# Kernel optimization log

Measured on AMD Instinct MI355X. Metric: run time of the kernel, lower is better.

Reference implementation:

```python
import jax, jax.numpy as jnp
import numpy as np

L, P = 16384, 512
DT_MIN, DT_MAX = 0.001, 0.1
THRESHOLD = 1.0  # spike threshold assumed for cartesian_spike


def setup_inputs() -> dict:
    key = jax.random.key(0)
    k1, k2, k3, k4, k5, k6 = jax.random.split(key, 6)
    u = jax.random.normal(k1, (L, P), dtype=jnp.float32)
    # Stored Lambda param: [..., 0] = log(-Re(Lambda)) with Re(Lambda) < 0, [..., 1] = Im(Lambda)
    lam_real_neg = jax.random.uniform(k2, (P,), minval=0.1, maxval=1.0)  # -Re(Lambda)
    lam_imag = jax.random.normal(k3, (P,)) * 3.0
    Lambda = jnp.stack([jnp.log(lam_real_neg), lam_imag], axis=-1).astype(jnp.float32)
    # init_log_steps: log(dt) uniform in [log(dt_min), log(dt_max)], shape (P, 1)
    log_step = (np.log(DT_MIN) + jax.random.uniform(k4, (P, 1)) * (np.log(DT_MAX) - np.log(DT_MIN))).astype(jnp.float32)
    V_re = jax.random.normal(k5, (P, P), dtype=jnp.float32) / np.sqrt(P)
    V_im = jax.random.normal(k6, (P, P), dtype=jnp.float32) / np.sqrt(P)
    return {"u": u, "Lambda": Lambda, "log_step": log_step, "V_re": V_re, "V_im": V_im}


def _binop(q_i, q_j):
    A_i, b_i = q_i
    A_j, b_j = q_j
    return (A_j * A_i, A_j * b_i + b_j)


def reference(u, Lambda, log_step, V_re, V_im):
    # keep_imag = False: u stays real. discretization = 'zoh', activation = 'cartesian_spike'.
    Lambda_tilde = -jnp.exp(Lambda[..., 0]) + 1j * Lambda[..., 1]            # (P,) complex
    step = jnp.exp(log_step[:, 0])                                            # (P,)
    Lambda_bar = jnp.exp(Lambda_tilde * step)                                 # (P,) |.|<1
    # B_tilde = I, so zoh gives B_bar = diag((Lambda_bar - 1)/Lambda); B_bar @ u_t = coef * u_t
    B_coef = (Lambda_bar - 1.0) / Lambda_tilde                                # (P,)
    Lambda_elements = jnp.broadcast_to(Lambda_bar, (u.shape[0], Lambda_bar.shape[0]))
    Bu_elements = B_coef[None, :] * u.astype(Lambda_bar.dtype)                # (L, P) complex
    _, xs = jax.lax.associative_scan(_binop, (Lambda_elements, Bu_elements))  # (L, P)
    V = V_re + 1j * V_im
    xs = xs @ V.T                                                             # vmap(V @ x) over L
    spikes = (xs.real > THRESHOLD).astype(jnp.float32)                        # cartesian_spike
    return spikes
```

## Files before the change

kernel.cpp:

```cpp
#include <hip/hip_runtime.h>

#define L_LEN   16384
#define P_DIM   512
#define CHUNK   64
#define NCHUNK  256

#define KDIM    1024
#define NDIM    512
#define BM      128
#define BN      128
#define BK      64

typedef __bf16 bf16_t;
typedef __bf16 bf16x8 __attribute__((ext_vector_type(8)));
typedef float  floatx4 __attribute__((ext_vector_type(4)));

__device__ __forceinline__ void channel_consts(const float* __restrict__ Lam,
                                               const float* __restrict__ lstep,
                                               int p, float& ar, float& ai,
                                               float& br, float& bi) {
    float lr = -expf(Lam[2 * p + 0]);
    float li = Lam[2 * p + 1];
    float s  = expf(lstep[p]);
    float er = expf(lr * s);
    ar = er * cosf(li * s);
    ai = er * sinf(li * s);
    float dr = ar - 1.0f, di = ai;
    float inv = 1.0f / (lr * lr + li * li);
    br = (dr * lr + di * li) * inv;
    bi = (di * lr - dr * li) * inv;
}

__global__ void __launch_bounds__(P_DIM) k_scan_ends(const float* __restrict__ u,
        const float* __restrict__ Lam, const float* __restrict__ lstep,
        float2* __restrict__ endv) {
    int p = threadIdx.x;
    int c = blockIdx.x;
    float ar, ai, br, bi;
    channel_consts(Lam, lstep, p, ar, ai, br, bi);
    float xr = 0.f, xi = 0.f;
    const float* up = u + (size_t)c * CHUNK * P_DIM + p;
    #pragma unroll 8
    for (int k = 0; k < CHUNK; ++k) {
        float uv = up[(size_t)k * P_DIM];
        float nr = ar * xr - ai * xi + br * uv;
        float ni = ar * xi + ai * xr + bi * uv;
        xr = nr; xi = ni;
    }
    endv[(size_t)c * P_DIM + p] = make_float2(xr, xi);
}

__global__ void __launch_bounds__(1024) k_carry(const float* __restrict__ Lam,
        const float* __restrict__ lstep, const float2* __restrict__ endv,
        float2* __restrict__ carry) {
    __shared__ float2 zl[4 * (NCHUNK + 2)];
    int tid = threadIdx.x;
    int g = tid & 3;
    int c = tid >> 2;
    int p = blockIdx.x * 4 + g;
    int zi_base = g * (NCHUNK + 2);

    float lr = -expf(Lam[2 * p + 0]);
    float li = Lam[2 * p + 1];
    float s  = expf(lstep[p]);
    float t  = s * (float)CHUNK;
    float er = expf(lr * t);
    float Ar = er * cosf(li * t);
    float Ai = er * sinf(li * t);

    float2 e = endv[(size_t)c * P_DIM + p];
    float zr = e.x, zi = e.y;
    zl[zi_base + c] = make_float2(zr, zi);
    __syncthreads();
    for (int st = 1; st < NCHUNK; st <<= 1) {
        float tr = 0.f, ti = 0.f;
        if (c >= st) { float2 v = zl[zi_base + c - st]; tr = v.x; ti = v.y; }
        __syncthreads();
        zr += Ar * tr - Ai * ti;
        zi += Ar * ti + Ai * tr;
        zl[zi_base + c] = make_float2(zr, zi);
        float nAr = Ar * Ar - Ai * Ai;
        float nAi = 2.f * Ar * Ai;
        Ar = nAr; Ai = nAi;
        __syncthreads();
    }
    float2 cv = make_float2(0.f, 0.f);
    if (c > 0) cv = zl[zi_base + c - 1];
    carry[(size_t)c * P_DIM + p] = cv;
}

__global__ void __launch_bounds__(P_DIM) k_materialize(const float* __restrict__ u,
        const float* __restrict__ Lam, const float* __restrict__ lstep,
        const float2* __restrict__ carry, bf16_t* __restrict__ A) {
    int p = threadIdx.x;
    int c = blockIdx.x;
    float ar, ai, br, bi;
    channel_consts(Lam, lstep, p, ar, ai, br, bi);
    float2 x0 = carry[(size_t)c * P_DIM + p];
    float xr = x0.x, xi = x0.y;
    const float* up = u + (size_t)c * CHUNK * P_DIM + p;
    uint32_t* Ap = (uint32_t*)(A + (size_t)c * CHUNK * KDIM) + p;
    #pragma unroll 4
    for (int k = 0; k < CHUNK; ++k) {
        float uv = up[(size_t)k * P_DIM];
        float nr = ar * xr - ai * xi + br * uv;
        float ni = ar * xi + ai * xr + bi * uv;
        xr = nr; xi = ni;
        bf16_t hr = (bf16_t)xr, hi = (bf16_t)xi;
        uint32_t pk = (uint32_t)__builtin_bit_cast(unsigned short, hr)
                    | ((uint32_t)__builtin_bit_cast(unsigned short, hi) << 16);
        Ap[(size_t)k * (KDIM / 2)] = pk;
    }
}

__global__ void __launch_bounds__(256) k_bt(const float* __restrict__ Vre,
        const float* __restrict__ Vim, bf16_t* __restrict__ Bt) {
    int idx = blockIdx.x * 256 + threadIdx.x;
    bf16_t r = (bf16_t)Vre[idx];
    bf16_t m = (bf16_t)(-Vim[idx]);
    uint32_t pk = (uint32_t)__builtin_bit_cast(unsigned short, r)
                | ((uint32_t)__builtin_bit_cast(unsigned short, m) << 16);
    ((uint32_t*)Bt)[idx] = pk;
}

__global__ void __launch_bounds__(256) k_gemm(const bf16_t* __restrict__ A,
        const bf16_t* __restrict__ Bt, float* __restrict__ out) {
    __shared__ uint4 As4[BM * BK * 2 / 16];
    __shared__ uint4 Bs4[BN * BK * 2 / 16];

    const int tid  = threadIdx.x;
    const int lane = tid & 63;
    const int w    = tid >> 6;
    const int m0   = blockIdx.x * BM;
    const int n0   = blockIdx.y * BN;
    const int wm   = (w >> 1) * 64;
    const int wn   = (w & 1) * 64;

    const int fr_m = lane & 15;
    const int fr_g = lane >> 4;

    floatx4 acc[4][4];
    #pragma unroll
    for (int i = 0; i < 4; ++i)
        #pragma unroll
        for (int j = 0; j < 4; ++j) {
            floatx4 z = {0.f, 0.f, 0.f, 0.f};
            acc[i][j] = z;
        }

    const bf16_t* Asrc = A  + (size_t)m0 * KDIM;
    const bf16_t* Bsrc = Bt + (size_t)n0 * KDIM;

    const bf16_t* ga[4]; const bf16_t* gb[4];
    char* la[4]; char* lb[4];
    #pragma unroll
    for (int i = 0; i < 4; ++i) {
        int q   = i * 256 + tid;
        int row = q >> 3;
        int gc  = (q & 7) ^ (row & 7);
        ga[i] = Asrc + (size_t)row * KDIM + gc * 8;
        gb[i] = Bsrc + (size_t)row * KDIM + gc * 8;
        la[i] = (char*)As4 + (size_t)q * 16;
        lb[i] = (char*)Bs4 + (size_t)q * 16;
    }

    for (int kt = 0; kt < KDIM; kt += BK) {
        __syncthreads();
        #pragma unroll
        for (int i = 0; i < 4; ++i) {
            __builtin_amdgcn_global_load_lds(
                (const __attribute__((address_space(1))) void*)(ga[i] + kt),
                (__attribute__((address_space(3))) void*)la[i], 16, 0, 0);
            __builtin_amdgcn_global_load_lds(
                (const __attribute__((address_space(1))) void*)(gb[i] + kt),
                (__attribute__((address_space(3))) void*)lb[i], 16, 0, 0);
        }
        __syncthreads();
        #pragma unroll
        for (int kk = 0; kk < BK; kk += 32) {
            bf16x8 af[4], bf[4];
            #pragma unroll
            for (int i = 0; i < 4; ++i) {
                int m  = wm + i * 16 + fr_m;
                int cc = (kk >> 3) + fr_g;
                int sc = cc ^ (m & 7);
                af[i] = *(const bf16x8*)((const bf16_t*)As4 + m * BK + sc * 8);
            }
            #pragma unroll
            for (int j = 0; j < 4; ++j) {
                int n  = wn + j * 16 + fr_m;
                int cc = (kk >> 3) + fr_g;
                int sc = cc ^ (n & 7);
                bf[j] = *(const bf16x8*)((const bf16_t*)Bs4 + n * BK + sc * 8);
            }
            #pragma unroll
            for (int i = 0; i < 4; ++i)
                #pragma unroll
                for (int j = 0; j < 4; ++j)
                    acc[i][j] = __builtin_amdgcn_mfma_f32_16x16x32_bf16(
                        af[i], bf[j], acc[i][j], 0, 0, 0);
        }
    }

    #pragma unroll
    for (int i = 0; i < 4; ++i)
        #pragma unroll
        for (int j = 0; j < 4; ++j)
            #pragma unroll
            for (int r = 0; r < 4; ++r) {
                int rr = wm + i * 16 + fr_g * 4 + r;
                int cl = wn + j * 16 + fr_m;
                float v = acc[i][j][r];
                out[(size_t)(m0 + rr) * NDIM + (n0 + cl)] = (v > 1.0f) ? 1.0f : 0.0f;
            }
}

extern "C" void kernel_launch(void* const* d_in, const int* in_sizes, int n_in,
                              void* d_out, int out_size, void* d_ws, size_t ws_size,
                              hipStream_t stream) {
    (void)in_sizes; (void)n_in; (void)out_size; (void)ws_size;
    const float* u     = (const float*)d_in[0];
    const float* Lam   = (const float*)d_in[1];
    const float* lstep = (const float*)d_in[2];
    const float* Vre   = (const float*)d_in[3];
    const float* Vim   = (const float*)d_in[4];
    float* out = (float*)d_out;

    char* ws = (char*)d_ws;
    const size_t endv_bytes  = (size_t)NCHUNK * P_DIM * sizeof(float2);
    const size_t carry_bytes = endv_bytes;
    const size_t bt_bytes    = (size_t)NDIM * KDIM * sizeof(bf16_t);
    float2* endv  = (float2*)(ws);
    float2* carry = (float2*)(ws + endv_bytes);
    bf16_t* Bt    = (bf16_t*)(ws + endv_bytes + carry_bytes);
    bf16_t* A     = (bf16_t*)(ws + endv_bytes + carry_bytes + bt_bytes);

    hipLaunchKernelGGL(k_scan_ends, dim3(NCHUNK), dim3(P_DIM), 0, stream,
                       u, Lam, lstep, endv);
    hipLaunchKernelGGL(k_bt, dim3(NDIM * P_DIM / 256), dim3(256), 0, stream,
                       Vre, Vim, Bt);
    hipLaunchKernelGGL(k_carry, dim3(P_DIM / 4), dim3(1024), 0, stream,
                       Lam, lstep, endv, carry);
    hipLaunchKernelGGL(k_materialize, dim3(NCHUNK), dim3(P_DIM), 0, stream,
                       u, Lam, lstep, carry, A);
    hipLaunchKernelGGL(k_gemm, dim3(L_LEN / BM, NDIM / BN), dim3(256), 0, stream,
                       A, Bt, out);
}
```

Baseline: 128.4 us.

## Fuse scan, carry, materialize and B prep into one cooperative kernel

Merges the chunk-end scan, the B-matrix bf16 packing, the cross-chunk carry propagation and the materialization into a single cooperative kernel that uses a grid-wide sync. The u chunk is held in registers so it is read once instead of twice. The log-depth shared-memory carry scan is replaced by a per-block serial loop over the preceding chunk ends. This removes three launches and one pass over u, but adds a grid barrier, a serial carry loop of up to 255 steps in later blocks, and heavy register use for the 64-element u buffer, which may lower occupancy.

Result: slower. 283.0 us (+120.4%).

```diff
diff --git a/kernel.cpp b/kernel.cpp
--- a/kernel.cpp
+++ b/kernel.cpp
@@ -1,4 +1,7 @@
 #include <hip/hip_runtime.h>
+#include <hip/hip_cooperative_groups.h>
+
+namespace cg = cooperative_groups;
 
 #define L_LEN   16384
 #define P_DIM   512
@@ -15,112 +18,77 @@
 typedef __bf16 bf16x8 __attribute__((ext_vector_type(8)));
 typedef float  floatx4 __attribute__((ext_vector_type(4)));
 
-__device__ __forceinline__ void channel_consts(const float* __restrict__ Lam,
-                                               const float* __restrict__ lstep,
-                                               int p, float& ar, float& ai,
-                                               float& br, float& bi) {
+__device__ __forceinline__ uint32_t pack_bf16(float a, float b) {
+    bf16_t ha = (bf16_t)a, hb = (bf16_t)b;
+    return (uint32_t)__builtin_bit_cast(unsigned short, ha)
+         | ((uint32_t)__builtin_bit_cast(unsigned short, hb) << 16);
+}
+
+__global__ void __launch_bounds__(P_DIM) k_scan_all(const float* __restrict__ u,
+        const float* __restrict__ Lam, const float* __restrict__ lstep,
+        const float* __restrict__ Vre, const float* __restrict__ Vim,
+        float2* __restrict__ endv, bf16_t* __restrict__ Bt,
+        bf16_t* __restrict__ A) {
+    const int p = threadIdx.x;
+    const int c = blockIdx.x;
+
+    {
+        int t = c * P_DIM + p;
+        float2 vr = ((const float2*)Vre)[t];
+        float2 vi = ((const float2*)Vim)[t];
+        uint2 pk = make_uint2(pack_bf16(vr.x, -vi.x), pack_bf16(vr.y, -vi.y));
+        ((uint2*)Bt)[t] = pk;
+    }
+
     float lr = -expf(Lam[2 * p + 0]);
     float li = Lam[2 * p + 1];
     float s  = expf(lstep[p]);
     float er = expf(lr * s);
-    ar = er * cosf(li * s);
-    ai = er * sinf(li * s);
+    float ar = er * cosf(li * s);
+    float ai = er * sinf(li * s);
     float dr = ar - 1.0f, di = ai;
     float inv = 1.0f / (lr * lr + li * li);
-    br = (dr * lr + di * li) * inv;
-    bi = (di * lr - dr * li) * inv;
-}
-
-__global__ void __launch_bounds__(P_DIM) k_scan_ends(const float* __restrict__ u,
-        const float* __restrict__ Lam, const float* __restrict__ lstep,
-        float2* __restrict__ endv) {
-    int p = threadIdx.x;
-    int c = blockIdx.x;
-    float ar, ai, br, bi;
-    channel_consts(Lam, lstep, p, ar, ai, br, bi);
+    float br = (dr * lr + di * li) * inv;
+    float bi = (di * lr - dr * li) * inv;
+    float tt = s * (float)CHUNK;
+    float eR = expf(lr * tt);
+    float Ar = eR * cosf(li * tt);
+    float Ai = eR * sinf(li * tt);
+
+    const float* up = u + (size_t)c * CHUNK * P_DIM + p;
+    float ur[CHUNK];
+    #pragma unroll
+    for (int k = 0; k < CHUNK; ++k) ur[k] = up[(size_t)k * P_DIM];
+
     float xr = 0.f, xi = 0.f;
-    const float* up = u + (size_t)c * CHUNK * P_DIM + p;
-    #pragma unroll 8
+    #pragma unroll
     for (int k = 0; k < CHUNK; ++k) {
-        float uv = up[(size_t)k * P_DIM];
-        float nr = ar * xr - ai * xi + br * uv;
-        float ni = ar * xi + ai * xr + bi * uv;
+        float nr = ar * xr - ai * xi + br * ur[k];
+        float ni = ar * xi + ai * xr + bi * ur[k];
         xr = nr; xi = ni;
     }
     endv[(size_t)c * P_DIM + p] = make_float2(xr, xi);
-}
-
-__global__ void __launch_bounds__(1024) k_carry(const float* __restrict__ Lam,
-        const float* __restrict__ lstep, const float2* __restrict__ endv,
-        float2* __restrict__ carry) {
-    __shared__ float2 zl[4 * (NCHUNK + 2)];
-    int tid = threadIdx.x;
-    int g = tid & 3;
-    int c = tid >> 2;
-    int p = blockIdx.x * 4 + g;
-    int zi_base = g * (NCHUNK + 2);
-
-    float lr = -expf(Lam[2 * p + 0]);
-    float li = Lam[2 * p + 1];
-    float s  = expf(lstep[p]);
-    float t  = s * (float)CHUNK;
-    float er = expf(lr * t);
-    float Ar = er * cosf(li * t);
-    float Ai = er * sinf(li * t);
-
-    float2 e = endv[(size_t)c * P_DIM + p];
-    float zr = e.x, zi = e.y;
-    zl[zi_base + c] = make_float2(zr, zi);
-    __syncthreads();
-    for (int st = 1; st < NCHUNK; st <<= 1) {
-        float tr = 0.f, ti = 0.f;
-        if (c >= st) { float2 v = zl[zi_base + c - st]; tr = v.x; ti = v.y; }
-        __syncthreads();
-        zr += Ar * tr - Ai * ti;
-        zi += Ar * ti + Ai * tr;
-        zl[zi_base + c] = make_float2(zr, zi);
-        float nAr = Ar * Ar - Ai * Ai;
-        float nAi = 2.f * Ar * Ai;
-        Ar = nAr; Ai = nAi;
-        __syncthreads();
-    }
-    float2 cv = make_float2(0.f, 0.f);
-    if (c > 0) cv = zl[zi_base + c - 1];
-    carry[(size_t)c * P_DIM + p] = cv;
-}
-
-__global__ void __launch_bounds__(P_DIM) k_materialize(const float* __restrict__ u,
-        const float* __restrict__ Lam, const float* __restrict__ lstep,
-        const float2* __restrict__ carry, bf16_t* __restrict__ A) {
-    int p = threadIdx.x;
-    int c = blockIdx.x;
-    float ar, ai, br, bi;
-    channel_consts(Lam, lstep, p, ar, ai, br, bi);
-    float2 x0 = carry[(size_t)c * P_DIM + p];
-    float xr = x0.x, xi = x0.y;
-    const float* up = u + (size_t)c * CHUNK * P_DIM + p;
+
+    __threadfence();
+    cg::this_grid().sync();
+
+    float cr = 0.f, ci = 0.f;
+    for (int j = 0; j < c; ++j) {
+        float2 e = endv[(size_t)j * P_DIM + p];
+        float nr = Ar * cr - Ai * ci + e.x;
+        float ni = Ar * ci + Ai * cr + e.y;
+        cr = nr; ci = ni;
+    }
+
+    xr = cr; xi = ci;
     uint32_t* Ap = (uint32_t*)(A + (size_t)c * CHUNK * KDIM) + p;
-    #pragma unroll 4
+    #pragma unroll
     for (int k = 0; k < CHUNK; ++k) {
-        float uv = up[(size_t)k * P_DIM];
-        float nr = ar * xr - ai * xi + br * uv;
-        float ni = ar * xi + ai * xr + bi * uv;
+        float nr = ar * xr - ai * xi + br * ur[k];
+        float ni = ar * xi + ai * xr + bi * ur[k];
         xr = nr; xi = ni;
-        bf16_t hr = (bf16_t)xr, hi = (bf16_t)xi;
-        uint32_t pk = (uint32_t)__builtin_bit_cast(unsigned short, hr)
-                    | ((uint32_t)__builtin_bit_cast(unsigned short, hi) << 16);
-        Ap[(size_t)k * (KDIM / 2)] = pk;
-    }
-}
-
-__global__ void __launch_bounds__(256) k_bt(const float* __restrict__ Vre,
-        const float* __restrict__ Vim, bf16_t* __restrict__ Bt) {
-    int idx = blockIdx.x * 256 + threadIdx.x;
-    bf16_t r = (bf16_t)Vre[idx];
-    bf16_t m = (bf16_t)(-Vim[idx]);
-    uint32_t pk = (uint32_t)__builtin_bit_cast(unsigned short, r)
-                | ((uint32_t)__builtin_bit_cast(unsigned short, m) << 16);
-    ((uint32_t*)Bt)[idx] = pk;
+        Ap[(size_t)k * (KDIM / 2)] = pack_bf16(xr, xi);
+    }
 }
 
 __global__ void __launch_bounds__(256) k_gemm(const bf16_t* __restrict__ A,
@@ -227,22 +195,17 @@
     float* out = (float*)d_out;
 
     char* ws = (char*)d_ws;
-    const size_t endv_bytes  = (size_t)NCHUNK * P_DIM * sizeof(float2);
-    const size_t carry_bytes = endv_bytes;
-    const size_t bt_bytes    = (size_t)NDIM * KDIM * sizeof(bf16_t);
-    float2* endv  = (float2*)(ws);
-    float2* carry = (float2*)(ws + endv_bytes);
-    bf16_t* Bt    = (bf16_t*)(ws + endv_bytes + carry_bytes);
-    bf16_t* A     = (bf16_t*)(ws + endv_bytes + carry_bytes + bt_bytes);
-
-    hipLaunchKernelGGL(k_scan_ends, dim3(NCHUNK), dim3(P_DIM), 0, stream,
-                       u, Lam, lstep, endv);
-    hipLaunchKernelGGL(k_bt, dim3(NDIM * P_DIM / 256), dim3(256), 0, stream,
-                       Vre, Vim, Bt);
-    hipLaunchKernelGGL(k_carry, dim3(P_DIM / 4), dim3(1024), 0, stream,
-                       Lam, lstep, endv, carry);
-    hipLaunchKernelGGL(k_materialize, dim3(NCHUNK), dim3(P_DIM), 0, stream,
-                       u, Lam, lstep, carry, A);
+    const size_t endv_bytes = (size_t)NCHUNK * P_DIM * sizeof(float2);
+    const size_t bt_bytes   = (size_t)NDIM * KDIM * sizeof(bf16_t);
+    float2* endv = (float2*)(ws);
+    bf16_t* Bt   = (bf16_t*)(ws + endv_bytes);
+    bf16_t* A    = (bf16_t*)(ws + endv_bytes + bt_bytes);
+
+    void* args[] = {(void*)&u, (void*)&Lam, (void*)&lstep, (void*)&Vre,
+                    (void*)&Vim, (void*)&endv, (void*)&Bt, (void*)&A};
+    hipLaunchCooperativeKernel((void*)k_scan_all, dim3(NCHUNK), dim3(P_DIM),
+                               args, 0, stream);
+
     hipLaunchKernelGGL(k_gemm, dim3(L_LEN / BM, NDIM / BN), dim3(256), 0, stream,
                        A, Bt, out);
 }
```
